# Kernel optimization log

Hardware: AMD Instinct MI355X
Metric: run time of the kernel (lower is better)

The kernel has to match this reference:

```python
import jax, jax.numpy as jnp
import numpy as np

N = 50000      # nodes
E = 500000     # edges
F = 128        # hidden_dim
NRBF = 20
CUTOFF = 5.0


def setup_inputs() -> dict:
    key = jax.random.key(0)
    ks = jax.random.split(key, 12)
    s = jax.random.normal(ks[0], (N, F), dtype=jnp.float32)
    v = jax.random.normal(ks[1], (N, 3, F), dtype=jnp.float32)
    pos = jax.random.normal(ks[2], (N, 3), dtype=jnp.float32)
    src = jax.random.randint(ks[3], (E,), 0, N)
    # avoid self-loops so rij never degenerates to exactly zero
    off = jax.random.randint(ks[4], (E,), 1, N)
    dst = (src + off) % N
    edge_index = jnp.stack([src, dst]).astype(jnp.int64)
    in_dim = 2 * F + NRBF
    sc = 0.02
    W1 = jax.random.normal(ks[5], (in_dim, 2 * F), dtype=jnp.float32) * sc
    b1 = jnp.zeros((2 * F,), dtype=jnp.float32)
    W2 = jax.random.normal(ks[6], (2 * F, 2 * F), dtype=jnp.float32) * sc
    b2 = jnp.zeros((2 * F,), dtype=jnp.float32)
    Ws = jax.random.normal(ks[7], (2 * F, F), dtype=jnp.float32) * sc
    bs = jnp.zeros((F,), dtype=jnp.float32)
    Wv = jax.random.normal(ks[8], (2 * F, F), dtype=jnp.float32) * sc
    bv = jnp.zeros((F,), dtype=jnp.float32)
    centers = jnp.linspace(0.0, CUTOFF, NRBF).astype(jnp.float32)
    delta = centers[1] - centers[0]
    widths = jnp.full((NRBF,), delta, dtype=jnp.float32)
    return {"s": s, "v": v, "pos": pos, "edge_index": edge_index,
            "W1": W1, "b1": b1, "W2": W2, "b2": b2,
            "Ws": Ws, "bs": bs, "Wv": Wv, "bv": bv,
            "centers": centers, "widths": widths}


def reference(s, v, pos, edge_index, W1, b1, W2, b2, Ws, bs, Wv, bv, centers, widths):
    src, dst = edge_index[0], edge_index[1]
    rij = pos[dst] - pos[src]                          # [E,3]
    dist = jnp.linalg.norm(rij, axis=-1, keepdims=True)  # [E,1]
    rbf = jnp.exp(-((dist - centers) / (widths + 1e-8)) ** 2)  # [E,NRBF]
    h = jnp.concatenate([s[src], s[dst], rbf], axis=-1)  # [E, 2F+NRBF]
    h = jax.nn.silu(h @ W1 + b1)
    h = jax.nn.silu(h @ W2 + b2)                         # [E, 2F]
    ds_edge = h @ Ws + bs                                # [E, F]
    dv_mag = h @ Wv + bv                                 # [E, F]
    safe = jnp.where(dist > 0, dist, 1.0)
    inv_dist = jnp.where(dist > 0, 1.0 / safe, 0.0)
    directions = rij * inv_dist                          # [E,3]
    dv_edge = directions[:, :, None] * dv_mag[:, None, :]  # [E,3,F]
    num_nodes = s.shape[0]
    ds = jax.ops.segment_sum(ds_edge, dst, num_segments=num_nodes)   # [N,F]
    dv = jax.ops.segment_sum(dv_edge, dst, num_segments=num_nodes)   # [N,3,F]
    return s + ds, v + dv
```

## Files before the change

### kernel.cpp

```cpp
#include <hip/hip_runtime.h>
#include <math.h>

#define FDIM   128
#define TWOF   256
#define NRBF_  20
#define INDIM  276
#define K1PAD  288
#define XS     296
#define TE     64

typedef __bf16 bf16x8 __attribute__((ext_vector_type(8)));
typedef __bf16 bf16x4 __attribute__((ext_vector_type(4)));
typedef float  f32x4  __attribute__((ext_vector_type(4)));
typedef float  f32x2  __attribute__((ext_vector_type(2)));
typedef unsigned int u32x4v __attribute__((ext_vector_type(4)));

__device__ inline float blo(unsigned p){ return __uint_as_float(p << 16); }
__device__ inline float bhi(unsigned p){ return __uint_as_float(p & 0xffff0000u); }


__global__ void sniff_idx(const int* __restrict__ ei, int nsample, int* __restrict__ flag) {
    __shared__ int any;
    if (threadIdx.x == 0) any = 0;
    __syncthreads();
    int nz = 0;
    for (int i = threadIdx.x; i < nsample; i += blockDim.x)
        nz |= (ei[2 * i + 1] != 0);
    if (nz) atomicOr(&any, 1);
    __syncthreads();
    if (threadIdx.x == 0) *flag = any;
}

__global__ void init_out(const float4* __restrict__ s4, const float4* __restrict__ v4,
                         float4* __restrict__ out4, int nf4, int total4) {
    for (int i = blockIdx.x * blockDim.x + threadIdx.x; i < total4;
         i += gridDim.x * blockDim.x)
        out4[i] = (i < nf4) ? s4[i] : v4[i - nf4];
}

__global__ void prep_weights(const float* __restrict__ W1, const float* __restrict__ W2,
                             const float* __restrict__ Ws, const float* __restrict__ Wv,
                             __bf16* __restrict__ W1t, __bf16* __restrict__ W2t,
                             __bf16* __restrict__ W3t) {
    int id = blockIdx.x * 256 + threadIdx.x;
    const int n1 = 256 * K1PAD;
    if (id < n1) {
        int n = id / K1PAD, k = id - n * K1PAD;
        W1t[id] = (k < INDIM) ? (__bf16)W1[k * TWOF + n] : (__bf16)0.f;
    } else if (id < n1 + 65536) {
        int j = id - n1; int n = j >> 8, k = j & 255;
        W2t[j] = (__bf16)W2[k * TWOF + n];
    } else if (id < n1 + 131072) {
        int j = id - n1 - 65536; int n = j >> 8, k = j & 255;
        W3t[j] = (n < FDIM) ? (__bf16)Ws[k * FDIM + n]
                            : (__bf16)Wv[k * FDIM + (n - FDIM)];
    }
}

__global__ void prep_s(const float4* __restrict__ s4, bf16x8* __restrict__ s16, int n8) {
    int i = blockIdx.x * 256 + threadIdx.x;
    if (i >= n8) return;
    float4 a = s4[i * 2], b = s4[i * 2 + 1];
    bf16x8 o;
    o[0] = (__bf16)a.x; o[1] = (__bf16)a.y; o[2] = (__bf16)a.z; o[3] = (__bf16)a.w;
    o[4] = (__bf16)b.x; o[5] = (__bf16)b.y; o[6] = (__bf16)b.z; o[7] = (__bf16)b.w;
    s16[i] = o;
}


__global__ void zero_hist(int* __restrict__ hist, int N) {
    int i = blockIdx.x * 256 + threadIdx.x;
    if (i < N) hist[i] = 0;
}

__global__ void hist_k(const int* __restrict__ ei, const int* __restrict__ flag,
                       int* __restrict__ hist, int E) {
    int e = blockIdx.x * 256 + threadIdx.x;
    if (e >= E) return;
    int dst = (*flag == 0) ? ei[2 * (E + e)] : ei[E + e];
    atomicAdd(&hist[dst], 1);
}

__global__ void scan_a(const int* __restrict__ hist, int* __restrict__ loc,
                       int* __restrict__ bsum, int N) {
    __shared__ int sums[256];
    int t = threadIdx.x;
    int base = blockIdx.x * 1024 + t * 4;
    int v0 = (base + 0 < N) ? hist[base + 0] : 0;
    int v1 = (base + 1 < N) ? hist[base + 1] : 0;
    int v2 = (base + 2 < N) ? hist[base + 2] : 0;
    int v3 = (base + 3 < N) ? hist[base + 3] : 0;
    int s = v0 + v1 + v2 + v3;
    sums[t] = s;
    __syncthreads();
    for (int off = 1; off < 256; off <<= 1) {
        int x = (t >= off) ? sums[t - off] : 0;
        __syncthreads();
        sums[t] += x;
        __syncthreads();
    }
    int excl = sums[t] - s;
    if (t == 255) bsum[blockIdx.x] = sums[255];
    if (base + 0 < N) loc[base + 0] = excl; excl += v0;
    if (base + 1 < N) loc[base + 1] = excl; excl += v1;
    if (base + 2 < N) loc[base + 2] = excl; excl += v2;
    if (base + 3 < N) loc[base + 3] = excl;
}

__global__ void scan_b(int* __restrict__ bsum, int nb) {
    if (threadIdx.x == 0 && blockIdx.x == 0) {
        int run = 0;
        for (int i = 0; i < nb; ++i) { int v = bsum[i]; bsum[i] = run; run += v; }
    }
}

__global__ void scan_c(const int* __restrict__ loc, const int* __restrict__ bsum,
                       int* __restrict__ rs, int* __restrict__ cursor, int N, int E) {
    int i = blockIdx.x * 256 + threadIdx.x;
    if (i < N) {
        int v = loc[i] + bsum[i >> 10];
        rs[i] = v; cursor[i] = v;
    }
    if (i == 0) rs[N] = E;
}

__global__ void scatter_k(const int* __restrict__ ei, const int* __restrict__ flag,
                          int* __restrict__ cursor, int* __restrict__ perm, int E) {
    int e = blockIdx.x * 256 + threadIdx.x;
    if (e >= E) return;
    int dst = (*flag == 0) ? ei[2 * (E + e)] : ei[E + e];
    int pos = atomicAdd(&cursor[dst], 1);
    perm[e] = pos;
}


template<int CSR>
__launch_bounds__(256, 4)
__global__ void edge_kernel(const __bf16* __restrict__ s16,
                            const float* __restrict__ pos,
                            const int* __restrict__ ei,
                            const float* __restrict__ b1, const float* __restrict__ b2,
                            const float* __restrict__ bsm, const float* __restrict__ bvm,
                            const float* __restrict__ centers, const float* __restrict__ widths,
                            const __bf16* __restrict__ W1t, const __bf16* __restrict__ W2t,
                            const __bf16* __restrict__ W3t,
                            const int* __restrict__ flag,
                            const int* __restrict__ perm,
                            __bf16* __restrict__ EO,
                            float* __restrict__ dirx, float* __restrict__ diry,
                            float* __restrict__ dirz,
                            float* __restrict__ out, int N, int E) {
    __shared__ __align__(16) __bf16 Sb[TE][XS];
    __shared__ float sdir[3][TE];
    __shared__ int ssrc[TE], sdst[TE], svalid[TE], sperm[TE];

    const int t    = threadIdx.x;
    const int lane = t & 63;
    const int wave = t >> 6;
    const int e0   = blockIdx.x * TE;
    const int i64  = (*flag == 0);

    {
        const int eL  = t >> 2;
        const int sub = t & 3;
        int e = e0 + eL;
        int valid = (e < E);
        int srcn = 0, dstn = 0;
        if (valid) {
            if (i64) { srcn = ei[2 * e]; dstn = ei[2 * (E + e)]; }
            else     { srcn = ei[e];     dstn = ei[E + e]; }
        }
        float rx = pos[dstn * 3 + 0] - pos[srcn * 3 + 0];
        float ry = pos[dstn * 3 + 1] - pos[srcn * 3 + 1];
        float rz = pos[dstn * 3 + 2] - pos[srcn * 3 + 2];
        float dist = sqrtf(rx * rx + ry * ry + rz * rz);
        if (sub == 0) {
            ssrc[eL] = srcn; sdst[eL] = dstn; svalid[eL] = valid;
            float inv = dist > 0.f ? 1.f / dist : 0.f;
            float dx = rx * inv, dy = ry * inv, dz = rz * inv;
            sdir[0][eL] = dx; sdir[1][eL] = dy; sdir[2][eL] = dz;
            int p = 0;
            if (CSR && valid) {
                p = perm[e];
                __builtin_nontemporal_store(dx, &dirx[p]);
                __builtin_nontemporal_store(dy, &diry[p]);
                __builtin_nontemporal_store(dz, &dirz[p]);
            }
            sperm[eL] = p;
        }
#pragma unroll
        for (int k8 = 0; k8 < 8; ++k8) {
            int k = sub * 8 + k8;
            float val = 0.f;
            if (k < NRBF_) {
                float u = (dist - centers[k]) / (widths[k] + 1e-8f);
                val = __expf(-u * u);
            }
            Sb[eL][TWOF + k] = (__bf16)val;
        }
    }
    __syncthreads();

    {
        const int pair = lane >> 5;
        const int half = (lane >> 4) & 1;
        const int q    = lane & 15;
        const bf16x8* s8 = (const bf16x8*)s16;
#pragma unroll
        for (int i = 0; i < 8; ++i) {
            int e = wave * 16 + i * 2 + pair;
            int node = half ? sdst[e] : ssrc[e];
            bf16x8 x = s8[node * 16 + q];
            *(bf16x8*)&Sb[e][half * FDIM + q * 8] = x;
        }
    }
    __syncthreads();

    const int l15 = lane & 15;
    const int kg  = (lane >> 4) * 8;
    const int nbase = wave * 64;

    f32x4 acc[4][4];

#pragma unroll
    for (int et = 0; et < 4; ++et)
#pragma unroll
        for (int nt = 0; nt < 4; ++nt) acc[et][nt] = (f32x4)0.f;
    {
        const __bf16* bp[4];
#pragma unroll
        for (int nt = 0; nt < 4; ++nt)
            bp[nt] = &W1t[(size_t)(nbase + nt * 16 + l15) * K1PAD + kg];
        bf16x8 bcur[4];
#pragma unroll
        for (int nt = 0; nt < 4; ++nt) bcur[nt] = *(const bf16x8*)bp[nt];
        __builtin_amdgcn_s_setprio(1);
#pragma unroll
        for (int kc = 0; kc < K1PAD; kc += 32) {
            bf16x8 bnxt[4];
            if (kc + 32 < K1PAD) {
#pragma unroll
                for (int nt = 0; nt < 4; ++nt)
                    bnxt[nt] = *(const bf16x8*)(bp[nt] + kc + 32);
            }
            bf16x8 a[4];
#pragma unroll
            for (int et = 0; et < 4; ++et)
                a[et] = *(const bf16x8*)&Sb[et * 16 + l15][kc + kg];
#pragma unroll
            for (int nt = 0; nt < 4; ++nt)
#pragma unroll
                for (int et = 0; et < 4; ++et)
                    acc[et][nt] = __builtin_amdgcn_mfma_f32_16x16x32_bf16(a[et], bcur[nt], acc[et][nt], 0, 0, 0);
#pragma unroll
            for (int nt = 0; nt < 4; ++nt) bcur[nt] = bnxt[nt];
        }
        __builtin_amdgcn_s_setprio(0);
    }
    __syncthreads();
#pragma unroll
    for (int nt = 0; nt < 4; ++nt) {
        int n = nbase + nt * 16 + l15;
        float bb = b1[n];
#pragma unroll
        for (int et = 0; et < 4; ++et)
#pragma unroll
            for (int r = 0; r < 4; ++r) {
                int m = et * 16 + (lane >> 4) * 4 + r;
                float h = acc[et][nt][r] + bb;
                Sb[m][n] = (__bf16)(h * __builtin_amdgcn_rcpf(1.f + __expf(-h)));
            }
    }
    __syncthreads();

#pragma unroll
    for (int et = 0; et < 4; ++et)
#pragma unroll
        for (int nt = 0; nt < 4; ++nt) acc[et][nt] = (f32x4)0.f;
    {
        const __bf16* bp[4];
#pragma unroll
        for (int nt = 0; nt < 4; ++nt)
            bp[nt] = &W2t[(size_t)(nbase + nt * 16 + l15) * TWOF + kg];
        bf16x8 bcur[4];
#pragma unroll
        for (int nt = 0; nt < 4; ++nt) bcur[nt] = *(const bf16x8*)bp[nt];
        __builtin_amdgcn_s_setprio(1);
#pragma unroll
        for (int kc = 0; kc < TWOF; kc += 32) {
            bf16x8 bnxt[4];
            if (kc + 32 < TWOF) {
#pragma unroll
                for (int nt = 0; nt < 4; ++nt)
                    bnxt[nt] = *(const bf16x8*)(bp[nt] + kc + 32);
            }
            bf16x8 a[4];
#pragma unroll
            for (int et = 0; et < 4; ++et)
                a[et] = *(const bf16x8*)&Sb[et * 16 + l15][kc + kg];
#pragma unroll
            for (int nt = 0; nt < 4; ++nt)
#pragma unroll
                for (int et = 0; et < 4; ++et)
                    acc[et][nt] = __builtin_amdgcn_mfma_f32_16x16x32_bf16(a[et], bcur[nt], acc[et][nt], 0, 0, 0);
#pragma unroll
            for (int nt = 0; nt < 4; ++nt) bcur[nt] = bnxt[nt];
        }
        __builtin_amdgcn_s_setprio(0);
    }
    __syncthreads();
#pragma unroll
    for (int nt = 0; nt < 4; ++nt) {
        int n = nbase + nt * 16 + l15;
        float bb = b2[n];
#pragma unroll
        for (int et = 0; et < 4; ++et)
#pragma unroll
            for (int r = 0; r < 4; ++r) {
                int m = et * 16 + (lane >> 4) * 4 + r;
                float h = acc[et][nt][r] + bb;
                Sb[m][n] = (__bf16)(h * __builtin_amdgcn_rcpf(1.f + __expf(-h)));
            }
    }
    __syncthreads();

#pragma unroll
    for (int et = 0; et < 4; ++et)
#pragma unroll
        for (int nt = 0; nt < 4; ++nt) acc[et][nt] = (f32x4)0.f;
    {
        const __bf16* bp[4];
#pragma unroll
        for (int nt = 0; nt < 4; ++nt) {
            int rowbase = ((nt >= 2) ? FDIM : 0) + wave * 32 + (nt & 1) * 16 + l15;
            bp[nt] = &W3t[(size_t)rowbase * TWOF + kg];
        }
        bf16x8 bcur[4];
#pragma unroll
        for (int nt = 0; nt < 4; ++nt) bcur[nt] = *(const bf16x8*)bp[nt];
        __builtin_amdgcn_s_setprio(1);
#pragma unroll
        for (int kc = 0; kc < TWOF; kc += 32) {
            bf16x8 bnxt[4];
            if (kc + 32 < TWOF) {
#pragma unroll
                for (int nt = 0; nt < 4; ++nt)
                    bnxt[nt] = *(const bf16x8*)(bp[nt] + kc + 32);
            }
            bf16x8 a[4];
#pragma unroll
            for (int et = 0; et < 4; ++et)
                a[et] = *(const bf16x8*)&Sb[et * 16 + l15][kc + kg];
#pragma unroll
            for (int nt = 0; nt < 4; ++nt)
#pragma unroll
                for (int et = 0; et < 4; ++et)
                    acc[et][nt] = __builtin_amdgcn_mfma_f32_16x16x32_bf16(a[et], bcur[nt], acc[et][nt], 0, 0, 0);
#pragma unroll
            for (int nt = 0; nt < 4; ++nt) bcur[nt] = bnxt[nt];
        }
        __builtin_amdgcn_s_setprio(0);
    }

    float b3v[4];
#pragma unroll
    for (int nt = 0; nt < 4; ++nt) {
        int n = wave * 32 + (nt & 1) * 16 + l15;
        b3v[nt] = (nt < 2) ? bsm[n] : bvm[n];
    }

    if (CSR) {
        __syncthreads();
        __bf16 (*EOs)[XS] = (__bf16(*)[XS])(&Sb[0][0]);
#pragma unroll
        for (int nt = 0; nt < 4; ++nt) {
            int col = ((nt >= 2) ? FDIM : 0) + wave * 32 + (nt & 1) * 16 + l15;
            float bb = b3v[nt];
#pragma unroll
            for (int et = 0; et < 4; ++et)
#pragma unroll
                for (int r = 0; r < 4; ++r) {
                    int m = et * 16 + (lane >> 4) * 4 + r;
                    EOs[m][col] = (__bf16)(acc[et][nt][r] + bb);
                }
        }
        __syncthreads();
        u32x4v* dst4 = (u32x4v*)EO;
#pragma unroll
        for (int j = 0; j < 8; ++j) {
            int flat = j * 256 + t;
            int row = flat >> 5, col = flat & 31;
            if (!svalid[row]) continue;
            __builtin_nontemporal_store(*(const u32x4v*)&EOs[row][col * 8],
                                        &dst4[(size_t)sperm[row] * 32 + col]);
        }
    } else {
        float* outs = out;
        float* outv = out + (size_t)N * FDIM;
#pragma unroll
        for (int et = 0; et < 4; ++et) {
#pragma unroll
            for (int r = 0; r < 4; ++r) {
                int m = et * 16 + (lane >> 4) * 4 + r;
                if (!svalid[m]) continue;
                int dst = sdst[m];
                float dx = sdir[0][m], dy = sdir[1][m], dz = sdir[2][m];
#pragma unroll
                for (int nt = 0; nt < 4; ++nt) {
                    int n = wave * 32 + (nt & 1) * 16 + l15;
                    float val = acc[et][nt][r] + b3v[nt];
                    if (nt < 2) {
                        atomicAdd(&outs[dst * FDIM + n], val);
                    } else {
                        int base = dst * 3 * FDIM + n;
                        atomicAdd(&outv[base],            dx * val);
                        atomicAdd(&outv[base + FDIM],     dy * val);
                        atomicAdd(&outv[base + 2 * FDIM], dz * val);
                    }
                }
            }
        }
    }
}


__launch_bounds__(256)
__global__ void node_kernel(const float* __restrict__ s, const float* __restrict__ v,
                            const __bf16* __restrict__ EO,
                            const float* __restrict__ dirx, const float* __restrict__ diry,
                            const float* __restrict__ dirz,
                            const int* __restrict__ rs,
                            float* __restrict__ out, int N) {
    int wave = threadIdx.x >> 6, lane = threadIdx.x & 63;
    int n = blockIdx.x * 4 + wave;
    if (n >= N) return;
    int beg = rs[n], end = rs[n + 1];

    float a0 = 0.f, a1 = 0.f;
    float vx0 = 0.f, vx1 = 0.f, vy0 = 0.f, vy1 = 0.f, vz0 = 0.f, vz1 = 0.f;
    const unsigned* EO32 = (const unsigned*)EO;

#pragma unroll 2
    for (int i = beg; i < end; ++i) {
        unsigned pds = __builtin_nontemporal_load(&EO32[(size_t)i * 128 + lane]);
        unsigned pvm = __builtin_nontemporal_load(&EO32[(size_t)i * 128 + 64 + lane]);
        float dx = __builtin_nontemporal_load(&dirx[i]);
        float dy = __builtin_nontemporal_load(&diry[i]);
        float dz = __builtin_nontemporal_load(&dirz[i]);
        float d0 = blo(pds), d1 = bhi(pds);
        float m0 = blo(pvm), m1 = bhi(pvm);
        a0 += d0; a1 += d1;
        vx0 = fmaf(dx, m0, vx0); vx1 = fmaf(dx, m1, vx1);
        vy0 = fmaf(dy, m0, vy0); vy1 = fmaf(dy, m1, vy1);
        vz0 = fmaf(dz, m0, vz0); vz1 = fmaf(dz, m1, vz1);
    }

    f32x2 sv = *((const f32x2*)&s[(size_t)n * FDIM] + lane);
    f32x2 o0 = { sv.x + a0, sv.y + a1 };
    __builtin_nontemporal_store(o0, (f32x2*)&out[(size_t)n * FDIM] + lane);

    const float* vb = &v[(size_t)n * 3 * FDIM];
    float* ovb = &out[(size_t)N * FDIM + (size_t)n * 3 * FDIM];
    f32x2 vv;
    vv = *((const f32x2*)vb + lane);
    f32x2 ox = { vv.x + vx0, vv.y + vx1 };
    __builtin_nontemporal_store(ox, (f32x2*)ovb + lane);
    vv = *((const f32x2*)(vb + FDIM) + lane);
    f32x2 oy = { vv.x + vy0, vv.y + vy1 };
    __builtin_nontemporal_store(oy, (f32x2*)(ovb + FDIM) + lane);
    vv = *((const f32x2*)(vb + 2 * FDIM) + lane);
    f32x2 oz = { vv.x + vz0, vv.y + vz1 };
    __builtin_nontemporal_store(oz, (f32x2*)(ovb + 2 * FDIM) + lane);
}


static inline size_t align256(size_t x) { return (x + 255) & ~(size_t)255; }

extern "C" void kernel_launch(void* const* d_in, const int* in_sizes, int n_in,
                              void* d_out, int out_size, void* d_ws, size_t ws_size,
                              hipStream_t stream) {
    const float* s   = (const float*)d_in[0];
    const float* v   = (const float*)d_in[1];
    const float* pos = (const float*)d_in[2];
    const int*   ei  = (const int*)d_in[3];
    const float* W1  = (const float*)d_in[4];
    const float* b1  = (const float*)d_in[5];
    const float* W2  = (const float*)d_in[6];
    const float* b2  = (const float*)d_in[7];
    const float* Wsm = (const float*)d_in[8];
    const float* bsm = (const float*)d_in[9];
    const float* Wvm = (const float*)d_in[10];
    const float* bvm = (const float*)d_in[11];
    const float* centers = (const float*)d_in[12];
    const float* widths  = (const float*)d_in[13];
    float* out = (float*)d_out;

    int N = in_sizes[0] / FDIM;
    int E = in_sizes[3] / 2;
    int nblocks = (E + TE - 1) / TE;

    size_t off = 0;
    int* flag = (int*)((char*)d_ws + off);           off = align256(off + 4);
    __bf16* W1t = (__bf16*)((char*)d_ws + off);      off = align256(off + (size_t)256 * K1PAD * 2);
    __bf16* W2t = (__bf16*)((char*)d_ws + off);      off = align256(off + (size_t)256 * TWOF * 2);
    __bf16* W3t = (__bf16*)((char*)d_ws + off);      off = align256(off + (size_t)256 * TWOF * 2);
    __bf16* s16 = (__bf16*)((char*)d_ws + off);      off = align256(off + (size_t)N * FDIM * 2);
    int* hist   = (int*)((char*)d_ws + off);         off = align256(off + (size_t)N * 4);
    int* loc    = (int*)((char*)d_ws + off);         off = align256(off + (size_t)N * 4);
    int* bsum   = (int*)((char*)d_ws + off);         off = align256(off + 1024);
    int* rs     = (int*)((char*)d_ws + off);         off = align256(off + (size_t)(N + 1) * 4);
    int* cursor = (int*)((char*)d_ws + off);         off = align256(off + (size_t)N * 4);
    int* perm   = (int*)((char*)d_ws + off);         off = align256(off + (size_t)E * 4);
    float* dirx = (float*)((char*)d_ws + off);       off = align256(off + (size_t)E * 4);
    float* diry = (float*)((char*)d_ws + off);       off = align256(off + (size_t)E * 4);
    float* dirz = (float*)((char*)d_ws + off);       off = align256(off + (size_t)E * 4);
    __bf16* EO  = (__bf16*)((char*)d_ws + off);      off = align256(off + (size_t)E * 256 * 2);
    bool use_csr = (off <= ws_size);

    int nsample = E < 1024 ? E : 1024;
    hipLaunchKernelGGL(sniff_idx, dim3(1), dim3(256), 0, stream, ei, nsample, flag);

    int nprep = 256 * K1PAD + 2 * 256 * TWOF;
    hipLaunchKernelGGL(prep_weights, dim3((nprep + 255) / 256), dim3(256), 0, stream,
                       W1, W2, Wsm, Wvm, W1t, W2t, W3t);

    int n8 = (N * FDIM) / 8;
    hipLaunchKernelGGL(prep_s, dim3((n8 + 255) / 256), dim3(256), 0, stream,
                       (const float4*)s, (bf16x8*)s16, n8);

    if (use_csr) {
        int nb = (N + 1023) / 1024;
        hipLaunchKernelGGL(zero_hist, dim3((N + 255) / 256), dim3(256), 0, stream, hist, N);
        hipLaunchKernelGGL(hist_k, dim3((E + 255) / 256), dim3(256), 0, stream, ei, flag, hist, E);
        hipLaunchKernelGGL(scan_a, dim3(nb), dim3(256), 0, stream, hist, loc, bsum, N);
        hipLaunchKernelGGL(scan_b, dim3(1), dim3(64), 0, stream, bsum, nb);
        hipLaunchKernelGGL(scan_c, dim3((N + 255) / 256), dim3(256), 0, stream, loc, bsum, rs, cursor, N, E);
        hipLaunchKernelGGL(scatter_k, dim3((E + 255) / 256), dim3(256), 0, stream, ei, flag, cursor, perm, E);

        hipLaunchKernelGGL(edge_kernel<1>, dim3(nblocks), dim3(256), 0, stream,
                           s16, pos, ei, b1, b2, bsm, bvm, centers, widths,
                           W1t, W2t, W3t, flag, perm, EO, dirx, diry, dirz, out, N, E);

        hipLaunchKernelGGL(node_kernel, dim3((N + 3) / 4), dim3(256), 0, stream,
                           s, v, EO, dirx, diry, dirz, rs, out, N);
    } else {
        int nf4    = (N * FDIM) / 4;
        int total4 = N * FDIM;
        hipLaunchKernelGGL(init_out, dim3(8192), dim3(256), 0, stream,
                           (const float4*)s, (const float4*)v, (float4*)out, nf4, total4);
        hipLaunchKernelGGL(edge_kernel<0>, dim3(nblocks), dim3(256), 0, stream,
                           s16, pos, ei, b1, b2, bsm, bvm, centers, widths,
                           W1t, W2t, W3t, flag, perm, EO, dirx, diry, dirz, out, N, E);
    }
}
```

Before: 711.9 us.

## Gather node features directly into swizzled LDS via global_load_lds

Replaces the register-staged gather of s[src]/s[dst] rows into a padded shared buffer with direct global-to-LDS loads, issued at kernel start before the geometry/RBF work so the gather overlaps it. The activation tile becomes an unpadded 256-wide XOR-swizzled layout, with the RBF features held in a separate small buffer used for the last K chunk of the first GEMM. This removes one barrier and the VGPR round-trip, and cuts LDS padding while avoiding bank conflicts through the swizzle. In exchange, all reads and writes now depend on hand-computed swizzle addressing, and tail edges clamp to the last valid index.

```diff
diff --git a/kernel.cpp b/kernel.cpp
--- a/kernel.cpp
+++ b/kernel.cpp
@@ -6,17 +6,21 @@
 #define NRBF_  20
 #define INDIM  276
 #define K1PAD  288
-#define XS     296
 #define TE     64
 
 typedef __bf16 bf16x8 __attribute__((ext_vector_type(8)));
-typedef __bf16 bf16x4 __attribute__((ext_vector_type(4)));
 typedef float  f32x4  __attribute__((ext_vector_type(4)));
 typedef float  f32x2  __attribute__((ext_vector_type(2)));
 typedef unsigned int u32x4v __attribute__((ext_vector_type(4)));
 
 __device__ inline float blo(unsigned p){ return __uint_as_float(p << 16); }
 __device__ inline float bhi(unsigned p){ return __uint_as_float(p & 0xffff0000u); }
+
+__device__ __forceinline__ void gload_lds16(const void* g, void* l) {
+    __builtin_amdgcn_global_load_lds(
+        (const __attribute__((address_space(1))) unsigned int*)g,
+        (__attribute__((address_space(3))) unsigned int*)l, 16, 0, 0);
+}
 
 
 __global__ void sniff_idx(const int* __restrict__ ei, int nsample, int* __restrict__ flag) {
@@ -150,7 +154,8 @@
                             float* __restrict__ dirx, float* __restrict__ diry,
                             float* __restrict__ dirz,
                             float* __restrict__ out, int N, int E) {
-    __shared__ __align__(16) __bf16 Sb[TE][XS];
+    __shared__ __align__(1024) __bf16 Xs[TE][256];
+    __shared__ __align__(16)   __bf16 Rb[TE][40];
     __shared__ float sdir[3][TE];
     __shared__ int ssrc[TE], sdst[TE], svalid[TE], sperm[TE];
 
@@ -159,6 +164,26 @@
     const int wave = t >> 6;
     const int e0   = blockIdx.x * TE;
     const int i64  = (*flag == 0);
+
+    {
+        const int j    = lane & 31;
+        const int rsel = lane >> 5;
+        int nd[8];
+#pragma unroll
+        for (int i = 0; i < 8; ++i) {
+            int eg = e0 + wave * 16 + 2 * i + rsel;
+            if (eg >= E) eg = E - 1;
+            int idx = (j < 16) ? eg : (E + eg);
+            nd[i] = i64 ? ei[2 * idx] : ei[idx];
+        }
+#pragma unroll
+        for (int i = 0; i < 8; ++i) {
+            int q = (j & 15) ^ ((2 * i + rsel) & 7);
+            const char* gp = (const char*)s16 + ((size_t)(unsigned)nd[i] << 8) + (q << 4);
+            char* lp = (char*)&Xs[wave * 16 + 2 * i][0];
+            gload_lds16(gp, lp);
+        }
+    }
 
     {
         const int eL  = t >> 2;
@@ -196,22 +221,7 @@
                 float u = (dist - centers[k]) / (widths[k] + 1e-8f);
                 val = __expf(-u * u);
             }
-            Sb[eL][TWOF + k] = (__bf16)val;
-        }
-    }
-    __syncthreads();
-
-    {
-        const int pair = lane >> 5;
-        const int half = (lane >> 4) & 1;
-        const int q    = lane & 15;
-        const bf16x8* s8 = (const bf16x8*)s16;
-#pragma unroll
-        for (int i = 0; i < 8; ++i) {
-            int e = wave * 16 + i * 2 + pair;
-            int node = half ? sdst[e] : ssrc[e];
-            bf16x8 x = s8[node * 16 + q];
-            *(bf16x8*)&Sb[e][half * FDIM + q * 8] = x;
+            Rb[eL][k] = (__bf16)val;
         }
     }
     __syncthreads();
@@ -219,6 +229,9 @@
     const int l15 = lane & 15;
     const int kg  = (lane >> 4) * 8;
     const int nbase = wave * 64;
+    const unsigned axor = (unsigned)((l15 & 7) << 4);
+    const char* xb = (const char*)&Xs[0][0] + l15 * 512;
+    char* xw = (char*)&Xs[0][0];
 
     f32x4 acc[4][4];
 
@@ -244,9 +257,15 @@
                     bnxt[nt] = *(const bf16x8*)(bp[nt] + kc + 32);
             }
             bf16x8 a[4];
-#pragma unroll
-            for (int et = 0; et < 4; ++et)
-                a[et] = *(const bf16x8*)&Sb[et * 16 + l15][kc + kg];
+            if (kc < 256) {
+#pragma unroll
+                for (int et = 0; et < 4; ++et)
+                    a[et] = *(const bf16x8*)(xb + et * 8192 + (((unsigned)((kc + kg) * 2)) ^ axor));
+            } else {
+#pragma unroll
+                for (int et = 0; et < 4; ++et)
+                    a[et] = *(const bf16x8*)&Rb[et * 16 + l15][kg];
+            }
 #pragma unroll
             for (int nt = 0; nt < 4; ++nt)
 #pragma unroll
@@ -268,7 +287,8 @@
             for (int r = 0; r < 4; ++r) {
                 int m = et * 16 + (lane >> 4) * 4 + r;
                 float h = acc[et][nt][r] + bb;
-                Sb[m][n] = (__bf16)(h * __builtin_amdgcn_rcpf(1.f + __expf(-h)));
+                *(__bf16*)(xw + m * 512 + (((unsigned)(n * 2)) ^ (((unsigned)(m & 7)) << 4)))
+                    = (__bf16)(h * __builtin_amdgcn_rcpf(1.f + __expf(-h)));
             }
     }
     __syncthreads();
@@ -297,7 +317,7 @@
             bf16x8 a[4];
 #pragma unroll
             for (int et = 0; et < 4; ++et)
-                a[et] = *(const bf16x8*)&Sb[et * 16 + l15][kc + kg];
+                a[et] = *(const bf16x8*)(xb + et * 8192 + (((unsigned)((kc + kg) * 2)) ^ axor));
 #pragma unroll
             for (int nt = 0; nt < 4; ++nt)
 #pragma unroll
@@ -319,7 +339,8 @@
             for (int r = 0; r < 4; ++r) {
                 int m = et * 16 + (lane >> 4) * 4 + r;
                 float h = acc[et][nt][r] + bb;
-                Sb[m][n] = (__bf16)(h * __builtin_amdgcn_rcpf(1.f + __expf(-h)));
+                *(__bf16*)(xw + m * 512 + (((unsigned)(n * 2)) ^ (((unsigned)(m & 7)) << 4)))
+                    = (__bf16)(h * __builtin_amdgcn_rcpf(1.f + __expf(-h)));
             }
     }
     __syncthreads();
@@ -350,7 +371,7 @@
             bf16x8 a[4];
 #pragma unroll
             for (int et = 0; et < 4; ++et)
-                a[et] = *(const bf16x8*)&Sb[et * 16 + l15][kc + kg];
+                a[et] = *(const bf16x8*)(xb + et * 8192 + (((unsigned)((kc + kg) * 2)) ^ axor));
 #pragma unroll
             for (int nt = 0; nt < 4; ++nt)
 #pragma unroll
@@ -371,7 +392,6 @@
 
     if (CSR) {
         __syncthreads();
-        __bf16 (*EOs)[XS] = (__bf16(*)[XS])(&Sb[0][0]);
 #pragma unroll
         for (int nt = 0; nt < 4; ++nt) {
             int col = ((nt >= 2) ? FDIM : 0) + wave * 32 + (nt & 1) * 16 + l15;
@@ -381,7 +401,8 @@
 #pragma unroll
                 for (int r = 0; r < 4; ++r) {
                     int m = et * 16 + (lane >> 4) * 4 + r;
-                    EOs[m][col] = (__bf16)(acc[et][nt][r] + bb);
+                    *(__bf16*)(xw + m * 512 + (((unsigned)(col * 2)) ^ (((unsigned)(m & 7)) << 4)))
+                        = (__bf16)(acc[et][nt][r] + bb);
                 }
         }
         __syncthreads();
@@ -389,10 +410,11 @@
 #pragma unroll
         for (int j = 0; j < 8; ++j) {
             int flat = j * 256 + t;
-            int row = flat >> 5, col = flat & 31;
+            int row = flat >> 5, slot = flat & 31;
             if (!svalid[row]) continue;
-            __builtin_nontemporal_store(*(const u32x4v*)&EOs[row][col * 8],
-                                        &dst4[(size_t)sperm[row] * 32 + col]);
+            u32x4v val = *(const u32x4v*)((const char*)&Xs[0][0] + row * 512
+                                          + ((slot ^ (row & 7)) << 4));
+            __builtin_nontemporal_store(val, &dst4[(size_t)sperm[row] * 32 + slot]);
         }
     } else {
         float* outs = out;
```

New measurement: 826.7 us. 16.1% more time.

## Merge prep kernels and gather node features before geometry to drop a barrier

Applied to the files above, without the earlier changes.

Folds the weight conversion, the bf16 conversion of s and the histogram zeroing into one prep_all launch, removing two kernel launches. In the edge kernel, the s[src]/s[dst] gather now reads indices straight from edge_index instead of shared memory, so it runs before the geometry/RBF stage and one __syncthreads is removed. This lets the feature gathers overlap the position loads, at the cost of reading the indices from global memory twice.

```diff
diff --git a/kernel.cpp b/kernel.cpp
--- a/kernel.cpp
+++ b/kernel.cpp
@@ -10,7 +10,6 @@
 #define TE     64
 
 typedef __bf16 bf16x8 __attribute__((ext_vector_type(8)));
-typedef __bf16 bf16x4 __attribute__((ext_vector_type(4)));
 typedef float  f32x4  __attribute__((ext_vector_type(4)));
 typedef float  f32x2  __attribute__((ext_vector_type(2)));
 typedef unsigned int u32x4v __attribute__((ext_vector_type(4)));
@@ -38,40 +37,37 @@
         out4[i] = (i < nf4) ? s4[i] : v4[i - nf4];
 }
 
-__global__ void prep_weights(const float* __restrict__ W1, const float* __restrict__ W2,
-                             const float* __restrict__ Ws, const float* __restrict__ Wv,
-                             __bf16* __restrict__ W1t, __bf16* __restrict__ W2t,
-                             __bf16* __restrict__ W3t) {
+__global__ void prep_all(const float* __restrict__ W1, const float* __restrict__ W2,
+                         const float* __restrict__ Ws, const float* __restrict__ Wv,
+                         __bf16* __restrict__ W1t, __bf16* __restrict__ W2t,
+                         __bf16* __restrict__ W3t,
+                         const float4* __restrict__ s4, bf16x8* __restrict__ s16o, int n8,
+                         int* __restrict__ hist, int N) {
     int id = blockIdx.x * 256 + threadIdx.x;
     const int n1 = 256 * K1PAD;
+    const int nW = n1 + 131072;
     if (id < n1) {
         int n = id / K1PAD, k = id - n * K1PAD;
         W1t[id] = (k < INDIM) ? (__bf16)W1[k * TWOF + n] : (__bf16)0.f;
     } else if (id < n1 + 65536) {
         int j = id - n1; int n = j >> 8, k = j & 255;
         W2t[j] = (__bf16)W2[k * TWOF + n];
-    } else if (id < n1 + 131072) {
+    } else if (id < nW) {
         int j = id - n1 - 65536; int n = j >> 8, k = j & 255;
         W3t[j] = (n < FDIM) ? (__bf16)Ws[k * FDIM + n]
                             : (__bf16)Wv[k * FDIM + (n - FDIM)];
-    }
-}
-
-__global__ void prep_s(const float4* __restrict__ s4, bf16x8* __restrict__ s16, int n8) {
-    int i = blockIdx.x * 256 + threadIdx.x;
-    if (i >= n8) return;
-    float4 a = s4[i * 2], b = s4[i * 2 + 1];
-    bf16x8 o;
-    o[0] = (__bf16)a.x; o[1] = (__bf16)a.y; o[2] = (__bf16)a.z; o[3] = (__bf16)a.w;
-    o[4] = (__bf16)b.x; o[5] = (__bf16)b.y; o[6] = (__bf16)b.z; o[7] = (__bf16)b.w;
-    s16[i] = o;
-}
-
-
-__global__ void zero_hist(int* __restrict__ hist, int N) {
-    int i = blockIdx.x * 256 + threadIdx.x;
-    if (i < N) hist[i] = 0;
-}
+    } else if (id < nW + n8) {
+        int i = id - nW;
+        float4 a = s4[i * 2], b = s4[i * 2 + 1];
+        bf16x8 o;
+        o[0] = (__bf16)a.x; o[1] = (__bf16)a.y; o[2] = (__bf16)a.z; o[3] = (__bf16)a.w;
+        o[4] = (__bf16)b.x; o[5] = (__bf16)b.y; o[6] = (__bf16)b.z; o[7] = (__bf16)b.w;
+        s16o[i] = o;
+    } else if (id < nW + n8 + N) {
+        hist[id - nW - n8] = 0;
+    }
+}
+
 
 __global__ void hist_k(const int* __restrict__ ei, const int* __restrict__ flag,
                        int* __restrict__ hist, int E) {
@@ -161,6 +157,23 @@
     const int i64  = (*flag == 0);
 
     {
+        const int pair = lane >> 5;
+        const int half = (lane >> 4) & 1;
+        const int q    = lane & 15;
+        const bf16x8* s8 = (const bf16x8*)s16;
+#pragma unroll
+        for (int i = 0; i < 8; ++i) {
+            int eL = wave * 16 + i * 2 + pair;
+            int e = e0 + eL;
+            int ec = (e < E) ? e : 0;
+            int idx = half ? (E + ec) : ec;
+            int node = i64 ? ei[2 * idx] : ei[idx];
+            bf16x8 x = s8[node * 16 + q];
+            *(bf16x8*)&Sb[eL][half * FDIM + q * 8] = x;
+        }
+    }
+
+    {
         const int eL  = t >> 2;
         const int sub = t & 3;
         int e = e0 + eL;
@@ -197,21 +210,6 @@
                 val = __expf(-u * u);
             }
             Sb[eL][TWOF + k] = (__bf16)val;
-        }
-    }
-    __syncthreads();
-
-    {
-        const int pair = lane >> 5;
-        const int half = (lane >> 4) & 1;
-        const int q    = lane & 15;
-        const bf16x8* s8 = (const bf16x8*)s16;
-#pragma unroll
-        for (int i = 0; i < 8; ++i) {
-            int e = wave * 16 + i * 2 + pair;
-            int node = half ? sdst[e] : ssrc[e];
-            bf16x8 x = s8[node * 16 + q];
-            *(bf16x8*)&Sb[e][half * FDIM + q * 8] = x;
         }
     }
     __syncthreads();
@@ -520,17 +518,14 @@
     int nsample = E < 1024 ? E : 1024;
     hipLaunchKernelGGL(sniff_idx, dim3(1), dim3(256), 0, stream, ei, nsample, flag);
 
-    int nprep = 256 * K1PAD + 2 * 256 * TWOF;
-    hipLaunchKernelGGL(prep_weights, dim3((nprep + 255) / 256), dim3(256), 0, stream,
-                       W1, W2, Wsm, Wvm, W1t, W2t, W3t);
-
     int n8 = (N * FDIM) / 8;
-    hipLaunchKernelGGL(prep_s, dim3((n8 + 255) / 256), dim3(256), 0, stream,
-                       (const float4*)s, (bf16x8*)s16, n8);
+    int nprep = 256 * K1PAD + 131072 + n8 + N;
+    hipLaunchKernelGGL(prep_all, dim3((nprep + 255) / 256), dim3(256), 0, stream,
+                       W1, W2, Wsm, Wvm, W1t, W2t, W3t,
+                       (const float4*)s, (bf16x8*)s16, n8, hist, N);
 
     if (use_csr) {
         int nb = (N + 1023) / 1024;
-        hipLaunchKernelGGL(zero_hist, dim3((N + 255) / 256), dim3(256), 0, stream, hist, N);
         hipLaunchKernelGGL(hist_k, dim3((E + 255) / 256), dim3(256), 0, stream, ei, flag, hist, E);
         hipLaunchKernelGGL(scan_a, dim3(nb), dim3(256), 0, stream, hist, loc, bsum, N);
         hipLaunchKernelGGL(scan_b, dim3(1), dim3(64), 0, stream, bsum, nb);
```

Result: faster. 696.9 us (-2.1%).
